# Kernel optimization log

Hardware: AMD Instinct MI355X
Metric: run time of the kernel (lower is better)

The kernel has to match this reference:

```python
import jax, jax.numpy as jnp
import numpy as np

HIDDEN = 4096
N_HEADS = 32
N_KV_HEADS = 8
HEAD_DIM = 128
ROPE_THETA = 1000000.0
EPS = 1e-06
B, T = 1, 2048


def apply_rope(inputs, position_ids, head_dim, theta):
    # inputs: [B, T, H, D], position_ids: [B, T]
    fraction = 2 * jnp.arange(0, head_dim // 2, dtype=jnp.float32) / head_dim
    timescale = jnp.power(theta, fraction)  # [D/2]
    x = (position_ids.astype(jnp.float32)[..., None] / timescale[None, None, :])[..., None, :]  # [B,T,1,D/2]
    sin, cos = jnp.sin(x), jnp.cos(x)
    a, b = jnp.split(inputs, 2, axis=-1)
    return jnp.concatenate([a * cos - b * sin, b * cos + a * sin], axis=-1).astype(inputs.dtype)


def rms_norm(x, weight, eps=EPS):
    rms = jnp.sqrt(jnp.mean(x * x, axis=-1, keepdims=True) + eps)
    return weight * x / rms


def setup_inputs() -> dict:
    key = jax.random.key(0)
    ks = jax.random.split(key, 8)
    lecun = lambda k, shape: jax.random.normal(k, shape, jnp.float32) / np.sqrt(shape[0])
    return {
        "x": jax.random.normal(ks[0], (B, T, HIDDEN), jnp.float32),
        "Wq": lecun(ks[1], (HIDDEN, N_HEADS * HEAD_DIM)),
        "Wk": lecun(ks[2], (HIDDEN, N_KV_HEADS * HEAD_DIM)),
        "Wv": lecun(ks[3], (HIDDEN, N_KV_HEADS * HEAD_DIM)),
        "Wo": lecun(ks[4], (N_HEADS * HEAD_DIM, HIDDEN)),
        "q_norm_w": 1.0 + 0.01 * jax.random.normal(ks[5], (HEAD_DIM,), jnp.float32),
        "k_norm_w": 1.0 + 0.01 * jax.random.normal(ks[6], (HEAD_DIM,), jnp.float32),
        "attention_mask": jnp.ones((B, T), jnp.int32),
        "positions": jnp.broadcast_to(jnp.arange(T, dtype=jnp.int32)[None, :], (B, T)),
    }


def reference(x, Wq, Wk, Wv, Wo, q_norm_w, k_norm_w, attention_mask, positions):
    b, t, _ = x.shape
    q = rms_norm((x @ Wq).reshape(b, t, N_HEADS, HEAD_DIM), q_norm_w)
    k = rms_norm((x @ Wk).reshape(b, t, N_KV_HEADS, HEAD_DIM), k_norm_w)
    v = (x @ Wv).reshape(b, t, N_KV_HEADS, HEAD_DIM)
    q = apply_rope(q, positions, HEAD_DIM, ROPE_THETA)
    k = apply_rope(k, positions, HEAD_DIM, ROPE_THETA)
    # prefill path: kv_cache is None -> causal attention, padding mask on keys
    attn = jax.nn.dot_product_attention(
        q, k, v,
        scale=1.0 / HEAD_DIM ** 0.5,
        mask=attention_mask[:, None, None, :].astype(bool),
        is_causal=True,
    )
    out = attn.reshape(b, t, N_HEADS * HEAD_DIM) @ Wo
    return out, (k, v)
```

## Files before the change

### kernel.cpp

```cpp
#include <hip/hip_runtime.h>


typedef __bf16 bf16;
typedef __bf16 bf16x8 __attribute__((ext_vector_type(8)));
typedef float  f32x4  __attribute__((ext_vector_type(4)));

#define MFMA16(a, b, c) __builtin_amdgcn_mfma_f32_16x16x32_bf16((a), (b), (c), 0, 0, 0)

__global__ __launch_bounds__(256) void detect_convert(
    const unsigned short* __restrict__ probe,
    const void* __restrict__ qw_raw, const void* __restrict__ kw_raw,
    int* __restrict__ flag, bf16* __restrict__ qwc, bf16* __restrict__ kwc) {
    __shared__ int cnt;
    if (threadIdx.x == 0) cnt = 0;
    __syncthreads();
    int local = 0;
    for (int i = 0; i < 4; ++i) {
        const unsigned short w = probe[(threadIdx.x * 4 + i) * 2];
        const int e = (w >> 7) & 0xFF;
        if (e >= 90 && e <= 140) ++local;
    }
    atomicAdd(&cnt, local);
    __syncthreads();
    const bool isbf16 = cnt >= 700;
    if (threadIdx.x == 0) *flag = isbf16 ? 1 : 0;
    const int t = threadIdx.x;
    if (t < 128)
        qwc[t] = isbf16 ? ((const bf16*)qw_raw)[t] : (bf16)((const float*)qw_raw)[t];
    else
        kwc[t - 128] = isbf16 ? ((const bf16*)kw_raw)[t - 128] : (bf16)((const float*)kw_raw)[t - 128];
}

__global__ __launch_bounds__(256) void convert_x(const void* __restrict__ xv,
                                                 bf16* __restrict__ xb,
                                                 const int* __restrict__ flag) {
    const size_t i8 = ((size_t)blockIdx.x * 256 + threadIdx.x) * 8;
    if (*flag) {
        *(bf16x8*)&xb[i8] = *(const bf16x8*)&((const bf16*)xv)[i8];
    } else {
        const f32x4 a = *(const f32x4*)&((const float*)xv)[i8];
        const f32x4 b = *(const f32x4*)&((const float*)xv)[i8 + 4];
        bf16x8 o;
#pragma unroll
        for (int e = 0; e < 4; ++e) { o[e] = (bf16)a[e]; o[e + 4] = (bf16)b[e]; }
        *(bf16x8*)&xb[i8] = o;
    }
}

#define GBM 128
#define GBN 128
#define GBK 64
#define GLD 72

__global__ __launch_bounds__(256) void gemm_nt(
    const bf16* __restrict__ A,
    const void* __restrict__ B1v, const void* __restrict__ B2v, const void* __restrict__ B3v,
    bf16* __restrict__ Cb1, float* __restrict__ Cf1,
    bf16* __restrict__ Cb2, float* __restrict__ Cf2,
    bf16* __restrict__ Cb3, float* __restrict__ Cf3,
    const int* __restrict__ flag, int K,
    int ldb1, int ldb2, int ldb3, int ldc1, int ldc2, int ldc3,
    int ns1, int ns2) {
    __shared__ __align__(16) bf16 As[2][GBM * GLD];
    __shared__ __align__(16) bf16 Bs[2][GBN * GLD];

    int id = blockIdx.y * gridDim.x + blockIdx.x;
    const int nwg = gridDim.x * gridDim.y;
    id = (id & 7) * (nwg >> 3) + (id >> 3);
    const int bx = id % (int)gridDim.x;
    const int by = id / (int)gridDim.x;

    const void* Bv;
    bf16* Cb;
    float* Cf;
    int n0, ldb, ldc;
    if (bx < ns1) {
        Bv = B1v; Cb = Cb1; Cf = Cf1; n0 = bx * GBN; ldb = ldb1; ldc = ldc1;
    } else if (bx < ns1 + ns2) {
        Bv = B2v; Cb = Cb2; Cf = Cf2; n0 = (bx - ns1) * GBN; ldb = ldb2; ldc = ldc2;
    } else {
        Bv = B3v; Cb = Cb3; Cf = Cf3; n0 = (bx - ns1 - ns2) * GBN; ldb = ldb3; ldc = ldc3;
    }
    const int m0 = by * GBM;

    const bool bBf16 = (*flag) != 0;
    const bf16*  Bb = (const bf16*)Bv;
    const float* Bf = (const float*)Bv;

    const int tid  = threadIdx.x;
    const int wave = tid >> 6;
    const int lane = tid & 63;
    const int l15  = lane & 15;
    const int quad = lane >> 4;
    const int wm = (wave >> 1) * 64;
    const int wn = (wave & 1) * 64;

    const int ar[4] = { (0 * 256 + tid) >> 3, (1 * 256 + tid) >> 3,
                        (2 * 256 + tid) >> 3, (3 * 256 + tid) >> 3 };
    const int ak = tid & 7;

    f32x4 acc[4][4];
#pragma unroll
    for (int i = 0; i < 4; ++i)
#pragma unroll
        for (int j = 0; j < 4; ++j) acc[i][j] = {0.f, 0.f, 0.f, 0.f};

    bf16x8 aReg[4];
    float  bRegF[4][8];
    bf16   bRegB[4][8];

#define LOAD_TILE(k0)                                                          \
    {                                                                          \
        _Pragma("unroll")                                                      \
        for (int p = 0; p < 4; ++p)                                            \
            aReg[p] = *(const bf16x8*)&A[(size_t)(m0 + ar[p]) * K + (k0) + ak * 8]; \
        if (bBf16) {                                                           \
            _Pragma("unroll")                                                  \
            for (int p = 0; p < 4; ++p) {                                      \
                const int w16 = wave * 4 + p;                                  \
                const int n = (w16 & 1) * 64 + lane, kc = w16 >> 1;            \
                _Pragma("unroll")                                              \
                for (int e = 0; e < 8; ++e)                                    \
                    bRegB[p][e] = Bb[(size_t)((k0) + kc * 8 + e) * ldb + n0 + n]; \
            }                                                                  \
        } else {                                                               \
            _Pragma("unroll")                                                  \
            for (int p = 0; p < 4; ++p) {                                      \
                const int w16 = wave * 4 + p;                                  \
                const int n = (w16 & 1) * 64 + lane, kc = w16 >> 1;            \
                _Pragma("unroll")                                              \
                for (int e = 0; e < 8; ++e)                                    \
                    bRegF[p][e] = Bf[(size_t)((k0) + kc * 8 + e) * ldb + n0 + n]; \
            }                                                                  \
        }                                                                      \
    }

#define WRITE_TILE(buf)                                                        \
    {                                                                          \
        _Pragma("unroll")                                                      \
        for (int p = 0; p < 4; ++p)                                            \
            *(bf16x8*)&As[buf][ar[p] * GLD + ak * 8] = aReg[p];                \
        _Pragma("unroll")                                                      \
        for (int p = 0; p < 4; ++p) {                                          \
            const int w16 = wave * 4 + p;                                      \
            const int n = (w16 & 1) * 64 + lane, kc = w16 >> 1;                \
            bf16x8 bv;                                                         \
            if (bBf16) {                                                       \
                _Pragma("unroll")                                              \
                for (int e = 0; e < 8; ++e) bv[e] = bRegB[p][e];               \
            } else {                                                           \
                _Pragma("unroll")                                              \
                for (int e = 0; e < 8; ++e) bv[e] = (bf16)bRegF[p][e];         \
            }                                                                  \
            *(bf16x8*)&Bs[buf][n * GLD + kc * 8] = bv;                         \
        }                                                                      \
    }

#define COMPUTE_TILE(buf)                                                      \
    {                                                                          \
        _Pragma("unroll")                                                      \
        for (int kk = 0; kk < GBK; kk += 32) {                                 \
            bf16x8 af[4], bfr[4];                                              \
            _Pragma("unroll")                                                  \
            for (int i = 0; i < 4; ++i)                                        \
                af[i] = *(const bf16x8*)&As[buf][(wm + i * 16 + l15) * GLD + kk + quad * 8]; \
            _Pragma("unroll")                                                  \
            for (int j = 0; j < 4; ++j)                                        \
                bfr[j] = *(const bf16x8*)&Bs[buf][(wn + j * 16 + l15) * GLD + kk + quad * 8]; \
            _Pragma("unroll")                                                  \
            for (int i = 0; i < 4; ++i)                                        \
                _Pragma("unroll")                                              \
                for (int j = 0; j < 4; ++j)                                    \
                    acc[i][j] = MFMA16(af[i], bfr[j], acc[i][j]);              \
        }                                                                      \
    }

    const int nt = K >> 6;
    LOAD_TILE(0);
    WRITE_TILE(0);
    __syncthreads();
    int cur = 0;
    for (int t = 0; t < nt; ++t) {
        if (t + 1 < nt) LOAD_TILE((t + 1) << 6);
        COMPUTE_TILE(cur);
        if (t + 1 < nt) {
            WRITE_TILE(cur ^ 1);
            __syncthreads();
        }
        cur ^= 1;
    }
#undef LOAD_TILE
#undef WRITE_TILE
#undef COMPUTE_TILE

#pragma unroll
    for (int i = 0; i < 4; ++i)
#pragma unroll
        for (int j = 0; j < 4; ++j)
#pragma unroll
            for (int r = 0; r < 4; ++r) {
                const int row = m0 + wm + i * 16 + quad * 4 + r;
                const int col = n0 + wn + j * 16 + l15;
                const float v = acc[i][j][r];
                if (Cb) Cb[(size_t)row * ldc + col] = (bf16)v;
                if (Cf) Cf[(size_t)row * ldc + col] = v;
            }
}

__global__ __launch_bounds__(256) void norm_rope(const bf16* __restrict__ src,
                                                 bf16* __restrict__ dst_bf,
                                                 float* __restrict__ dst_f32,
                                                 const bf16* __restrict__ w,
                                                 const int* __restrict__ positions,
                                                 int H) {
    const int wid  = blockIdx.x * 4 + (threadIdx.x >> 6);
    const int lane = threadIdx.x & 63;
    const int token = wid / H, head = wid % H;
    const bf16* s = src + ((size_t)token * H + head) * 128;
    const float f0 = (float)s[lane], f1 = (float)s[lane + 64];
    float ss = f0 * f0 + f1 * f1;
    for (int off = 32; off >= 1; off >>= 1) ss += __shfl_xor(ss, off);
    const float inv_rms = rsqrtf(ss * (1.0f / 128.0f) + 1e-6f);
    const float n0 = f0 * inv_rms * (float)w[lane];
    const float n1 = f1 * inv_rms * (float)w[lane + 64];
    const float pos = (float)positions[token];
    const float inv_ts = expf((float)lane * (-13.815510557964274f / 64.0f));
    const float ang = pos * inv_ts;
    const float sn = sinf(ang), cs = cosf(ang);
    const float o0 = n0 * cs - n1 * sn;
    const float o1 = n1 * cs + n0 * sn;
    const size_t base = ((size_t)token * H + head) * 128;
    if (dst_bf)  { dst_bf[base + lane] = (bf16)o0;  dst_bf[base + lane + 64] = (bf16)o1; }
    if (dst_f32) { dst_f32[base + lane] = o0;       dst_f32[base + lane + 64] = o1; }
}

__global__ __launch_bounds__(256) void flash_attn(const bf16* __restrict__ Q,
                                                  const bf16* __restrict__ Kg,
                                                  const bf16* __restrict__ Vg,
                                                  bf16* __restrict__ Og) {
    __shared__ __align__(16) bf16 Ks[32 * 128];
    __shared__ __align__(16) bf16 Vt[128 * 40];
    __shared__ __align__(16) bf16 Ps[4][16 * 40];

    int id = blockIdx.y * 32 + blockIdx.x;
    id = (id & 7) * 128 + (id >> 3);
    const int h  = id >> 5;
    const int qt = 31 - (id & 31);
    const int kvh  = h >> 2;
    const int tid  = threadIdx.x;
    const int wave = tid >> 6;
    const int lane = tid & 63;
    const int l15  = lane & 15;
    const int quad = lane >> 4;
    const int q0   = qt * 64;
    const int qw0  = q0 + wave * 16;
    const int myq  = qw0 + l15;
    const float scale = 0.08838834764831845f;

    bf16x8 qf[4];
    {
        const bf16* qrow = Q + ((size_t)myq * 32 + h) * 128;
#pragma unroll
        for (int kc = 0; kc < 4; ++kc)
            qf[kc] = *(const bf16x8*)&qrow[kc * 32 + quad * 8];
    }

    f32x4 oacc[8];
#pragma unroll
    for (int i = 0; i < 8; ++i) oacc[i] = {0.f, 0.f, 0.f, 0.f};
    float m_run = -1e30f, l_run = 0.f;

    const int ksr  = tid & 31;
    const int kscb = tid >> 5;
    const int vr0  = (tid & 15) * 2;
    const int vcb  = tid >> 4;

    char* kbytes = (char*)Ks;
    char* vbytes = (char*)Vt;
    char* pbytes = (char*)&Ps[wave][0];

    const int ntiles = (q0 + 64) >> 5;
    for (int kt = 0; kt < ntiles; ++kt) {
        const int kb = kt * 32;
        {
            const bf16* src = Kg + ((size_t)(kb + ksr) * 8 + kvh) * 128;
            const bf16x8 v0 = *(const bf16x8*)&src[kscb * 8];
            const bf16x8 v1 = *(const bf16x8*)&src[(kscb + 8) * 8];
            const int b0 = (ksr * 256 + kscb * 16) ^ ((ksr & 7) << 4);
            const int b1 = (ksr * 256 + (kscb + 8) * 16) ^ ((ksr & 7) << 4);
            *(bf16x8*)(kbytes + b0) = v0;
            *(bf16x8*)(kbytes + b1) = v1;
        }
        {
            const bf16* s0 = Vg + ((size_t)(kb + vr0) * 8 + kvh) * 128 + vcb * 8;
            const bf16x8 a = *(const bf16x8*)s0;
            const bf16x8 b = *(const bf16x8*)(s0 + 1024);
#pragma unroll
            for (int e = 0; e < 8; ++e) {
                union { bf16 hh[2]; unsigned int u; } pk;
                pk.hh[0] = a[e]; pk.hh[1] = b[e];
                *(unsigned int*)(vbytes + (vcb * 8 + e) * 80 + vr0 * 2) = pk.u;
            }
        }
        __syncthreads();

        f32x4 sacc[2];
        sacc[0] = {0.f, 0.f, 0.f, 0.f};
        sacc[1] = {0.f, 0.f, 0.f, 0.f};
#pragma unroll
        for (int st = 0; st < 2; ++st) {
            const int row = st * 16 + l15;
#pragma unroll
            for (int kc = 0; kc < 4; ++kc) {
                const int bofs = (row * 256 + kc * 64 + quad * 16) ^ ((row & 7) << 4);
                const bf16x8 kf = *(const bf16x8*)(kbytes + bofs);
                sacc[st] = MFMA16(kf, qf[kc], sacc[st]);
            }
        }

        float sv[8];
        float pm = -1e30f;
#pragma unroll
        for (int st = 0; st < 2; ++st)
#pragma unroll
            for (int r = 0; r < 4; ++r) {
                const int key = kb + st * 16 + quad * 4 + r;
                float s = sacc[st][r] * scale;
                if (key > myq) s = -1e30f;
                sv[st * 4 + r] = s;
                pm = fmaxf(pm, s);
            }
        pm = fmaxf(pm, __shfl_xor(pm, 16));
        pm = fmaxf(pm, __shfl_xor(pm, 32));
        const float m_new = fmaxf(m_run, pm);
        const float corr = __expf(m_run - m_new);
        float ps = 0.f;
        bf16 pb[8];
#pragma unroll
        for (int i = 0; i < 8; ++i) {
            const float p = __expf(sv[i] - m_new);
            ps += p;
            pb[i] = (bf16)p;
        }
        ps += __shfl_xor(ps, 16);
        ps += __shfl_xor(ps, 32);
        l_run = l_run * corr + ps;
        m_run = m_new;

#pragma unroll
        for (int st = 0; st < 2; ++st)
#pragma unroll
            for (int r = 0; r < 4; ++r)
                *(bf16*)(pbytes + l15 * 80 + (st * 16 + quad * 4 + r) * 2) = pb[st * 4 + r];

        float corrq[4];
#pragma unroll
        for (int r = 0; r < 4; ++r) corrq[r] = __shfl(corr, quad * 4 + r);
#pragma unroll
        for (int nt = 0; nt < 8; ++nt)
#pragma unroll
            for (int r = 0; r < 4; ++r) oacc[nt][r] *= corrq[r];

        const bf16x8 pf = *(const bf16x8*)(pbytes + l15 * 80 + quad * 16);
#pragma unroll
        for (int nt = 0; nt < 8; ++nt) {
            const bf16x8 vf = *(const bf16x8*)(vbytes + (nt * 16 + l15) * 80 + quad * 16);
            oacc[nt] = MFMA16(pf, vf, oacc[nt]);
        }
        __syncthreads();
    }

    const float rinv = 1.0f / l_run;
    float linv[4];
#pragma unroll
    for (int r = 0; r < 4; ++r) linv[r] = __shfl(rinv, quad * 4 + r);
#pragma unroll
    for (int nt = 0; nt < 8; ++nt)
#pragma unroll
        for (int r = 0; r < 4; ++r) {
            const int row = qw0 + quad * 4 + r;
            Og[((size_t)row * 32 + h) * 128 + nt * 16 + l15] = (bf16)(oacc[nt][r] * linv[r]);
        }
}

extern "C" void kernel_launch(void* const* d_in, const int* in_sizes, int n_in,
                              void* d_out, int out_size, void* d_ws, size_t ws_size,
                              hipStream_t stream) {
    const void* x  = d_in[0];
    const void* Wq = d_in[1];
    const void* Wk = d_in[2];
    const void* Wv = d_in[3];
    const void* Wo = d_in[4];
    const void* qw = d_in[5];
    const void* kw = d_in[6];
    const int* positions = (const int*)d_in[8];

    char* ws = (char*)d_ws;
    int*  flag    = (int*)ws;
    bf16* qwc     = (bf16*)(ws + 64);
    bf16* kwc     = (bf16*)(ws + 64 + 256);
    bf16* kq      = (bf16*)(ws + 4096);
    bf16* vb      = (bf16*)(ws + 4096 + 4194304);
    bf16* xb      = (bf16*)(ws + 4096 + 8388608);
    bf16* attnbuf = (bf16*)(ws + 4096 + 8388608);

    float* outf = (float*)d_out;
    float* Kof  = outf + 8388608;
    float* Vof  = outf + 10485760;
    bf16*  qb   = (bf16*)d_out;

    detect_convert<<<1, 256, 0, stream>>>((const unsigned short*)Wq, qw, kw, flag, qwc, kwc);
    convert_x<<<4096, 256, 0, stream>>>(x, xb, flag);

    gemm_nt<<<dim3(48, 16), 256, 0, stream>>>(
        xb, Wq, Wk, Wv,
        qb, nullptr, kq, nullptr, vb, Vof,
        flag, 4096,
        4096, 1024, 1024, 4096, 1024, 1024,
        32, 8);

    norm_rope<<<16384, 256, 0, stream>>>(qb, qb, nullptr, qwc, positions, 32);
    norm_rope<<<4096, 256, 0, stream>>>(kq, kq, Kof, kwc, positions, 8);

    flash_attn<<<dim3(32, 32), 256, 0, stream>>>(qb, kq, vb, attnbuf);

    gemm_nt<<<dim3(32, 16), 256, 0, stream>>>(
        attnbuf, Wo, Wo, Wo,
        nullptr, outf, nullptr, nullptr, nullptr, nullptr,
        flag, 4096,
        4096, 4096, 4096, 4096, 4096, 4096,
        32, 0);
}
```

Before: 697.7 us.

## Prefetch two K tiles ahead in GEMM and remap blocks per XCD

The GEMM main loop is unrolled by two and alternates between two register staging sets, so global loads for tile t+2 are issued while tile t is being computed. The fp32 weights are now converted to bf16 as they are loaded, which shrinks the staging registers needed for that extra depth. The block-to-XCD mapping changes so each XCD handles a contiguous group of column tiles across all row tiles, meant to improve weight reuse in each XCD's L2. In exchange the kernel uses more registers, which may reduce occupancy, and the mapping assumes the grid width is a multiple of eight.

```diff
diff --git a/kernel.cpp b/kernel.cpp
--- a/kernel.cpp
+++ b/kernel.cpp
@@ -64,11 +64,14 @@
     __shared__ __align__(16) bf16 As[2][GBM * GLD];
     __shared__ __align__(16) bf16 Bs[2][GBN * GLD];
 
+    {
+    }
+    const int nbxp = (int)gridDim.x >> 3;
     int id = blockIdx.y * gridDim.x + blockIdx.x;
-    const int nwg = gridDim.x * gridDim.y;
-    id = (id & 7) * (nwg >> 3) + (id >> 3);
-    const int bx = id % (int)gridDim.x;
-    const int by = id / (int)gridDim.x;
+    const int xcd = id & 7;
+    const int j = id >> 3;
+    const int bx = xcd * nbxp + j / (int)gridDim.y;
+    const int by = j % (int)gridDim.y;
 
     const void* Bv;
     bf16* Cb;
@@ -103,17 +106,16 @@
 #pragma unroll
     for (int i = 0; i < 4; ++i)
 #pragma unroll
-        for (int j = 0; j < 4; ++j) acc[i][j] = {0.f, 0.f, 0.f, 0.f};
-
-    bf16x8 aReg[4];
-    float  bRegF[4][8];
-    bf16   bRegB[4][8];
-
-#define LOAD_TILE(k0)                                                          \
+        for (int j2 = 0; j2 < 4; ++j2) acc[i][j2] = {0.f, 0.f, 0.f, 0.f};
+
+    bf16x8 aR0[4], aR1[4];
+    bf16   bR0[4][8], bR1[4][8];
+
+#define LOAD_TILE(k0, aR, bR)                                                  \
     {                                                                          \
         _Pragma("unroll")                                                      \
         for (int p = 0; p < 4; ++p)                                            \
-            aReg[p] = *(const bf16x8*)&A[(size_t)(m0 + ar[p]) * K + (k0) + ak * 8]; \
+            aR[p] = *(const bf16x8*)&A[(size_t)(m0 + ar[p]) * K + (k0) + ak * 8]; \
         if (bBf16) {                                                           \
             _Pragma("unroll")                                                  \
             for (int p = 0; p < 4; ++p) {                                      \
@@ -121,7 +123,7 @@
                 const int n = (w16 & 1) * 64 + lane, kc = w16 >> 1;            \
                 _Pragma("unroll")                                              \
                 for (int e = 0; e < 8; ++e)                                    \
-                    bRegB[p][e] = Bb[(size_t)((k0) + kc * 8 + e) * ldb + n0 + n]; \
+                    bR[p][e] = Bb[(size_t)((k0) + kc * 8 + e) * ldb + n0 + n]; \
             }                                                                  \
         } else {                                                               \
             _Pragma("unroll")                                                  \
@@ -130,28 +132,23 @@
                 const int n = (w16 & 1) * 64 + lane, kc = w16 >> 1;            \
                 _Pragma("unroll")                                              \
                 for (int e = 0; e < 8; ++e)                                    \
-                    bRegF[p][e] = Bf[(size_t)((k0) + kc * 8 + e) * ldb + n0 + n]; \
+                    bR[p][e] = (bf16)Bf[(size_t)((k0) + kc * 8 + e) * ldb + n0 + n]; \
             }                                                                  \
         }                                                                      \
     }
 
-#define WRITE_TILE(buf)                                                        \
+#define WRITE_TILE(buf, aR, bR)                                                \
     {                                                                          \
         _Pragma("unroll")                                                      \
         for (int p = 0; p < 4; ++p)                                            \
-            *(bf16x8*)&As[buf][ar[p] * GLD + ak * 8] = aReg[p];                \
+            *(bf16x8*)&As[buf][ar[p] * GLD + ak * 8] = aR[p];                  \
         _Pragma("unroll")                                                      \
         for (int p = 0; p < 4; ++p) {                                          \
             const int w16 = wave * 4 + p;                                      \
             const int n = (w16 & 1) * 64 + lane, kc = w16 >> 1;                \
             bf16x8 bv;                                                         \
-            if (bBf16) {                                                       \
-                _Pragma("unroll")                                              \
-                for (int e = 0; e < 8; ++e) bv[e] = bRegB[p][e];               \
-            } else {                                                           \
-                _Pragma("unroll")                                              \
-                for (int e = 0; e < 8; ++e) bv[e] = (bf16)bRegF[p][e];         \
-            }                                                                  \
+            _Pragma("unroll")                                                  \
+            for (int e = 0; e < 8; ++e) bv[e] = bR[p][e];                      \
             *(bf16x8*)&Bs[buf][n * GLD + kc * 8] = bv;                         \
         }                                                                      \
     }
@@ -165,30 +162,34 @@
             for (int i = 0; i < 4; ++i)                                        \
                 af[i] = *(const bf16x8*)&As[buf][(wm + i * 16 + l15) * GLD + kk + quad * 8]; \
             _Pragma("unroll")                                                  \
-            for (int j = 0; j < 4; ++j)                                        \
-                bfr[j] = *(const bf16x8*)&Bs[buf][(wn + j * 16 + l15) * GLD + kk + quad * 8]; \
+            for (int j3 = 0; j3 < 4; ++j3)                                     \
+                bfr[j3] = *(const bf16x8*)&Bs[buf][(wn + j3 * 16 + l15) * GLD + kk + quad * 8]; \
             _Pragma("unroll")                                                  \
             for (int i = 0; i < 4; ++i)                                        \
                 _Pragma("unroll")                                              \
-                for (int j = 0; j < 4; ++j)                                    \
-                    acc[i][j] = MFMA16(af[i], bfr[j], acc[i][j]);              \
+                for (int j3 = 0; j3 < 4; ++j3)                                 \
+                    acc[i][j3] = MFMA16(af[i], bfr[j3], acc[i][j3]);           \
         }                                                                      \
     }
 
     const int nt = K >> 6;
-    LOAD_TILE(0);
-    WRITE_TILE(0);
+    LOAD_TILE(0, aR0, bR0);
+    WRITE_TILE(0, aR0, bR0);
     __syncthreads();
-    int cur = 0;
-    for (int t = 0; t < nt; ++t) {
-        if (t + 1 < nt) LOAD_TILE((t + 1) << 6);
-        COMPUTE_TILE(cur);
-        if (t + 1 < nt) {
-            WRITE_TILE(cur ^ 1);
+    if (nt > 1) LOAD_TILE(1 << 6, aR1, bR1);
+    for (int t = 0; t + 2 <= nt; t += 2) {
+        if (t + 2 < nt) LOAD_TILE((t + 2) << 6, aR0, bR0);
+        COMPUTE_TILE(0);
+        WRITE_TILE(1, aR1, bR1);
+        __syncthreads();
+        if (t + 3 < nt) LOAD_TILE((t + 3) << 6, aR1, bR1);
+        COMPUTE_TILE(1);
+        if (t + 2 < nt) {
+            WRITE_TILE(0, aR0, bR0);
             __syncthreads();
         }
-        cur ^= 1;
-    }
+    }
+    if (nt & 1) COMPUTE_TILE(0);
 #undef LOAD_TILE
 #undef WRITE_TILE
 #undef COMPUTE_TILE
@@ -196,12 +197,12 @@
 #pragma unroll
     for (int i = 0; i < 4; ++i)
 #pragma unroll
-        for (int j = 0; j < 4; ++j)
+        for (int j2 = 0; j2 < 4; ++j2)
 #pragma unroll
             for (int r = 0; r < 4; ++r) {
                 const int row = m0 + wm + i * 16 + quad * 4 + r;
-                const int col = n0 + wn + j * 16 + l15;
-                const float v = acc[i][j][r];
+                const int col = n0 + wn + j2 * 16 + l15;
+                const float v = acc[i][j2][r];
                 if (Cb) Cb[(size_t)row * ldc + col] = (bf16)v;
                 if (Cf) Cf[(size_t)row * ldc + col] = v;
             }
```

After: 874.2 us. +25.3%, slower.
